# Performance work log

Hardware: AMD Instinct MI355X
Metric: run time of the kernel (lower is better)

The kernel has to match this reference:

```python
import jax, jax.numpy as jnp
import numpy as np

N = 80000   # active voxels
G = 64      # voxel grid side
K = 27      # 3x3x3 kernel taps


def _build_coord_maps():
    """Random unique voxel coords in a G^3 grid; 27-tap neighbor index map (-1 = missing)."""
    rng = np.random.default_rng(0)
    flat = rng.choice(G ** 3, size=N, replace=False).astype(np.int64)
    coords = np.stack(np.unravel_index(flat, (G, G, G)), axis=1)  # (N,3)
    order = np.argsort(flat)
    skeys = flat[order]
    offs = [(dx, dy, dz) for dx in (-1, 0, 1) for dy in (-1, 0, 1) for dz in (-1, 0, 1)]
    nbr = np.full((K, N), -1, np.int32)
    for k, (dx, dy, dz) in enumerate(offs):
        nc = coords + np.array([dx, dy, dz])
        inb = np.all((nc >= 0) & (nc < G), axis=1)
        nkey = nc[:, 0] * G * G + nc[:, 1] * G + nc[:, 2]
        pos = np.clip(np.searchsorted(skeys, nkey), 0, N - 1)
        hit = inb & (skeys[pos] == nkey)
        nbr[k] = np.where(hit, order[pos], -1)
    return nbr


_W_SPECS = [('a1w', (27, 96, 64)), ('a2w', (64, 64)), ('a3w', (27, 64, 64)), ('a4w', (64, 64)),
            ('b1w', (27, 256, 64)), ('b2w', (64, 64)), ('b3w', (27, 64, 32)), ('b4w', (32, 32)),
            ('c1w', (27, 96, 128)), ('c2w', (128, 128)), ('c3w', (128, 128))]
_BN_SPECS = [('a1', 64), ('a2', 64), ('a3', 64), ('a4', 64),
             ('b1', 64), ('b2', 64), ('b3', 32), ('b4', 32),
             ('c1', 128), ('c2', 128), ('c3', 128)]


def setup_inputs() -> dict:
    key = jax.random.key(0)
    ks = jax.random.split(key, 64)
    inp = {
        'feat3d': jax.random.normal(ks[0], (N, 96), jnp.float32),
        'feat2d': jax.random.normal(ks[1], (N, 256), jnp.float32),
    }
    i = 2
    for name, shp in _W_SPECS:
        fan = float(np.prod(shp[:-1]))
        inp[name] = jax.random.normal(ks[i], shp, jnp.float32) * (1.0 / np.sqrt(fan))
        i += 1
    for pre, c in _BN_SPECS:  # folded eval-mode BN: y = x*scale + shift
        inp[pre + 's'] = 1.0 + 0.1 * jax.random.normal(ks[i], (c,), jnp.float32)
        inp[pre + 'b'] = 0.1 * jax.random.normal(ks[i + 1], (c,), jnp.float32)
        i += 2
    inp['nbr_idx'] = jnp.asarray(_build_coord_maps())
    inp['align_idx'] = jnp.arange(N, dtype=jnp.int32)  # 2D/3D share coordinates -> exact match
    return inp


def _sconv(x, W, nbr):
    """Sparse 3x3x3 conv: per-tap masked gather + GEMM, accumulated (gather-GEMM-scatter)."""
    out = jnp.zeros((x.shape[0], W.shape[-1]), x.dtype)
    for k in range(W.shape[0]):
        idx = nbr[k]
        g = jnp.where((idx >= 0)[:, None], x[jnp.maximum(idx, 0)], 0.0)
        out = out + g @ W[k]
    return out


def _bnrelu(x, s, b):
    return jax.nn.relu(x * s + b)


def reference(feat3d, feat2d,
              a1w, a2w, a3w, a4w, b1w, b2w, b3w, b4w, c1w, c2w, c3w,
              a1s, a1b, a2s, a2b, a3s, a3b, a4s, a4b,
              b1s, b1b, b2s, b2b, b3s, b3b, b4s, b4b,
              c1s, c1b, c2s, c2b, c3s, c3b,
              nbr_idx, align_idx):
    # 3D branch: 96 -> 64 (dropout = identity in eval)
    x = _bnrelu(_sconv(feat3d, a1w, nbr_idx), a1s, a1b)
    x = _bnrelu(x @ a2w, a2s, a2b)
    x = _bnrelu(_sconv(x, a3w, nbr_idx), a3s, a3b)
    x3 = _bnrelu(x @ a4w, a4s, a4b)
    # 2D branch: 256 -> 32
    y = _bnrelu(_sconv(feat2d, b1w, nbr_idx), b1s, b1b)
    y = _bnrelu(y @ b2w, b2s, b2b)
    y = _bnrelu(_sconv(y, b3w, nbr_idx), b3s, b3b)
    y2 = _bnrelu(y @ b4w, b4s, b4b)
    # features_at_coordinates: exact-match gather at the 3D coords, NaN/Inf -> 0
    ya = y2[align_idx]
    ya = jnp.where(jnp.isfinite(ya), ya, 0.0)
    # fusion: concat 64+32=96 -> 128
    z = jnp.concatenate([x3, ya], axis=1)
    z = _bnrelu(_sconv(z, c1w, nbr_idx), c1s, c1b)
    z = _bnrelu(z @ c2w, c2s, c2b)
    z = _bnrelu(z @ c3w, c3s, c3b)
    return z
```

## Files before the change

### kernel.cpp

```cpp
#include <hip/hip_runtime.h>

typedef __bf16 bf16;
typedef __bf16 bf16x8 __attribute__((ext_vector_type(8)));
typedef __bf16 bf16x4 __attribute__((ext_vector_type(4)));
typedef float  f32x4  __attribute__((ext_vector_type(4)));

__global__ void f2b_kernel(const float* __restrict__ src, bf16* __restrict__ dst, int n4) {
    int i = blockIdx.x * 256 + threadIdx.x;
    if (i >= n4) return;
    float4 v = ((const float4*)src)[i];
    bf16x4 o = { (bf16)v.x, (bf16)v.y, (bf16)v.z, (bf16)v.w };
    ((bf16x4*)dst)[i] = o;
}

__global__ void swz_kernel(const float* __restrict__ W, bf16* __restrict__ Wf,
                           int cin, int cout, int total) {
    int e = blockIdx.x * 256 + threadIdx.x;
    if (e >= total) return;
    int per_tap = cin * cout;
    int tap = e / per_tap;
    int t2  = e - tap * per_tap;
    int ntc = cout >> 4;
    int s   = t2 / (ntc * 512);
    int r3  = t2 - s * (ntc * 512);
    int nt  = r3 >> 9;
    int L   = (r3 & 511) >> 3;
    int j   = r3 & 7;
    int k   = s * 32 + (L >> 4) * 8 + j;
    int col = nt * 16 + (L & 15);
    Wf[e] = (bf16)W[((size_t)tap * cin + k) * cout + col];
}

template<int CIN, int C1, int TAPS, int KTILE, int C2, int C3>
__global__ __launch_bounds__(256) void layer_kernel(
    const bf16* __restrict__ X,
    const bf16* __restrict__ W1,
    const bf16* __restrict__ W2,
    const bf16* __restrict__ W3,
    const int*  __restrict__ nbr,
    const float* __restrict__ sc1, const float* __restrict__ sh1,
    const float* __restrict__ sc2, const float* __restrict__ sh2,
    const float* __restrict__ sc3, const float* __restrict__ sh3,
    bf16* __restrict__ Y, float* __restrict__ Yf,
    int ystride, int yoff, int n, int nblocks)
{
    constexpr int NT1  = C1 / 16;
    constexpr int KH   = CIN / KTILE;
    constexpr int KS   = KTILE / 32;
    constexpr int CH   = KTILE / 8;
    constexpr int SREG = KTILE / 32;
    constexpr int AST  = KTILE + 8;
    constexpr int WR1  = (C1 >= 64) ? 2 : 1;
    constexpr int WC1  = (C1 == 128) ? 4 : 2;
    constexpr int RG1  = 4 / WR1;
    constexpr int ABUF = 64 * AST;
    constexpr int ABY  = 2 * ABUF * 2;
    constexpr int LS1  = C1 + 8;
    constexpr int LS2  = C2 + 8;
    constexpr int L1BY = 64 * LS1 * 2;
    constexpr int L2BY = (C3 > 0) ? 64 * LS2 * 2 : 0;
    constexpr int SBY  = (ABY > L1BY ? (ABY > L2BY ? ABY : L2BY)
                                     : (L1BY > L2BY ? L1BY : L2BY));

    __shared__ __align__(16) char smem[SBY];
    __shared__ int idxs[TAPS * 64];
    bf16* As = (bf16*)smem;

    const int tid = threadIdx.x;

    {
    }
    const int bq  = nblocks >> 3, br = nblocks & 7;
    const int bx  = blockIdx.x & 7, bs = blockIdx.x >> 3;
    const int sb  = bx * bq + (bx < br ? bx : br) + bs;
    const int base = sb * 64;

    const int lane  = tid & 63;
    const int wv    = tid >> 6;
    const int m16   = lane & 15;
    const int quad  = lane >> 4;
    const int wrow1 = wv % RG1;
    const int wcol1 = wv / RG1;

    for (int e = tid; e < TAPS * 64; e += 256)
        idxs[e] = nbr[(e >> 6) * n + base + (e & 63)];
    __syncthreads();

    int rr[SREG], cof[SREG], lofs[SREG];
#pragma unroll
    for (int j = 0; j < SREG; ++j) {
        int e = tid + 256 * j;
        rr[j]   = e / CH;
        int c   = e - rr[j] * CH;
        cof[j]  = c * 8;
        lofs[j] = rr[j] * AST + c * 8;
    }

    float4 sreg[SREG];
    auto issue_loads = [&](int kh, int t) {
#pragma unroll
        for (int j = 0; j < SREG; ++j) {
            int idx = idxs[t * 64 + rr[j]];
            float4 val = {0.f, 0.f, 0.f, 0.f};
            if (idx >= 0) val = *(const float4*)(X + (size_t)idx * CIN + kh * KTILE + cof[j]);
            sreg[j] = val;
        }
    };
    auto store_lds = [&](int buf) {
#pragma unroll
        for (int j = 0; j < SREG; ++j)
            *(float4*)(&As[buf * ABUF + lofs[j]]) = sreg[j];
    };

    f32x4 acc1[WR1][WC1];
#pragma unroll
    for (int r = 0; r < WR1; ++r)
#pragma unroll
        for (int c = 0; c < WC1; ++c) acc1[r][c] = (f32x4){0.f, 0.f, 0.f, 0.f};

    issue_loads(0, 0);
    store_lds(0);

    int it = 0;
    for (int kh = 0; kh < KH; ++kh)
        for (int t = 0; t < TAPS; ++t, ++it) {
            __syncthreads();

            const bf16* wt = W1 + (size_t)t * (CIN * C1);
            bf16x8 bfr[KS][WC1];
#pragma unroll
            for (int s = 0; s < KS; ++s)
#pragma unroll
                for (int c = 0; c < WC1; ++c)
                    bfr[s][c] = *(const bf16x8*)(wt + ((kh * KS + s) * NT1 + wcol1 * WC1 + c) * 512 + lane * 8);

            int t2 = t + 1, kh2 = kh;
            if (t2 == TAPS) { t2 = 0; kh2 = kh + 1; }
            const bool more = (kh2 < KH);
            if (more) issue_loads(kh2, t2);

            const int buf = it & 1;
#pragma unroll
            for (int s = 0; s < KS; ++s) {
                bf16x8 a[WR1];
#pragma unroll
                for (int r = 0; r < WR1; ++r)
                    a[r] = *(const bf16x8*)(&As[buf * ABUF + ((wrow1 * WR1 + r) * 16 + m16) * AST + s * 32 + quad * 8]);
#pragma unroll
                for (int r = 0; r < WR1; ++r)
#pragma unroll
                    for (int c = 0; c < WC1; ++c)
                        acc1[r][c] = __builtin_amdgcn_mfma_f32_16x16x32_bf16(a[r], bfr[s][c], acc1[r][c], 0, 0, 0);
            }

            if (more) store_lds(buf ^ 1);
        }

    __syncthreads();
    bf16* Lt1 = (bf16*)smem;
#pragma unroll
    for (int c = 0; c < WC1; ++c) {
        int col = (wcol1 * WC1 + c) * 16 + m16;
        float s1 = sc1[col], h1 = sh1[col];
#pragma unroll
        for (int r = 0; r < WR1; ++r) {
            int row0 = (wrow1 * WR1 + r) * 16 + quad * 4;
#pragma unroll
            for (int i = 0; i < 4; ++i) {
                float v = acc1[r][c][i] * s1 + h1;
                v = v > 0.f ? v : 0.f;
                Lt1[(row0 + i) * LS1 + col] = (bf16)v;
            }
        }
    }
    __syncthreads();

    constexpr int NT2 = C2 / 16;
    constexpr int WR2 = (C2 >= 64) ? 2 : 1;
    constexpr int WC2 = (C2 == 128) ? 4 : 2;
    constexpr int RG2 = 4 / WR2;
    constexpr int KS2 = C1 / 32;
    const int wrow2 = wv % RG2, wcol2 = wv / RG2;

    f32x4 acc2[WR2][WC2];
#pragma unroll
    for (int r = 0; r < WR2; ++r)
#pragma unroll
        for (int c = 0; c < WC2; ++c) acc2[r][c] = (f32x4){0.f, 0.f, 0.f, 0.f};

#pragma unroll
    for (int s = 0; s < KS2; ++s) {
        bf16x8 a[WR2], bw[WC2];
#pragma unroll
        for (int r = 0; r < WR2; ++r)
            a[r] = *(const bf16x8*)(&Lt1[((wrow2 * WR2 + r) * 16 + m16) * LS1 + s * 32 + quad * 8]);
#pragma unroll
        for (int c = 0; c < WC2; ++c)
            bw[c] = *(const bf16x8*)(W2 + ((s * NT2 + wcol2 * WC2 + c) * 512 + lane * 8));
#pragma unroll
        for (int r = 0; r < WR2; ++r)
#pragma unroll
            for (int c = 0; c < WC2; ++c)
                acc2[r][c] = __builtin_amdgcn_mfma_f32_16x16x32_bf16(a[r], bw[c], acc2[r][c], 0, 0, 0);
    }

    if constexpr (C3 == 0) {
#pragma unroll
        for (int c = 0; c < WC2; ++c) {
            int col = (wcol2 * WC2 + c) * 16 + m16;
            float s2 = sc2[col], h2 = sh2[col];
#pragma unroll
            for (int r = 0; r < WR2; ++r) {
                int row0 = base + (wrow2 * WR2 + r) * 16 + quad * 4;
#pragma unroll
                for (int i = 0; i < 4; ++i) {
                    float v = acc2[r][c][i] * s2 + h2;
                    v = v > 0.f ? v : 0.f;
                    size_t off = (size_t)(row0 + i) * ystride + yoff + col;
                    if (Yf) Yf[off] = v;
                    else    Y[off] = (bf16)v;
                }
            }
        }
    } else {
        __syncthreads();
        bf16* Lt2 = (bf16*)smem;
#pragma unroll
        for (int c = 0; c < WC2; ++c) {
            int col = (wcol2 * WC2 + c) * 16 + m16;
            float s2 = sc2[col], h2 = sh2[col];
#pragma unroll
            for (int r = 0; r < WR2; ++r) {
                int row0 = (wrow2 * WR2 + r) * 16 + quad * 4;
#pragma unroll
                for (int i = 0; i < 4; ++i) {
                    float v = acc2[r][c][i] * s2 + h2;
                    v = v > 0.f ? v : 0.f;
                    Lt2[(row0 + i) * LS2 + col] = (bf16)v;
                }
            }
        }
        __syncthreads();

        constexpr int C3v = (C3 > 0) ? C3 : 16;
        constexpr int NT3 = C3v / 16;
        constexpr int WR3 = (C3v >= 64) ? 2 : 1;
        constexpr int WC3 = (C3v == 128) ? 4 : 2;
        constexpr int RG3 = 4 / WR3;
        constexpr int KS3 = C2 / 32;
        const int wrow3 = wv % RG3, wcol3 = wv / RG3;

        f32x4 acc3[WR3][WC3];
#pragma unroll
        for (int r = 0; r < WR3; ++r)
#pragma unroll
            for (int c = 0; c < WC3; ++c) acc3[r][c] = (f32x4){0.f, 0.f, 0.f, 0.f};

#pragma unroll
        for (int s = 0; s < KS3; ++s) {
            bf16x8 a[WR3], bw[WC3];
#pragma unroll
            for (int r = 0; r < WR3; ++r)
                a[r] = *(const bf16x8*)(&Lt2[((wrow3 * WR3 + r) * 16 + m16) * LS2 + s * 32 + quad * 8]);
#pragma unroll
            for (int c = 0; c < WC3; ++c)
                bw[c] = *(const bf16x8*)(W3 + ((s * NT3 + wcol3 * WC3 + c) * 512 + lane * 8));
#pragma unroll
            for (int r = 0; r < WR3; ++r)
#pragma unroll
                for (int c = 0; c < WC3; ++c)
                    acc3[r][c] = __builtin_amdgcn_mfma_f32_16x16x32_bf16(a[r], bw[c], acc3[r][c], 0, 0, 0);
        }

#pragma unroll
        for (int c = 0; c < WC3; ++c) {
            int col = (wcol3 * WC3 + c) * 16 + m16;
            float s3 = sc3[col], h3 = sh3[col];
#pragma unroll
            for (int r = 0; r < WR3; ++r) {
                int row0 = base + (wrow3 * WR3 + r) * 16 + quad * 4;
#pragma unroll
                for (int i = 0; i < 4; ++i) {
                    float v = acc3[r][c][i] * s3 + h3;
                    v = v > 0.f ? v : 0.f;
                    size_t off = (size_t)(row0 + i) * ystride + yoff + col;
                    if (Yf) Yf[off] = v;
                    else    Y[off] = (bf16)v;
                }
            }
        }
    }
}

__global__ void concat_kernel(const bf16* __restrict__ y2, const int* __restrict__ align,
                              bf16* __restrict__ z, int n) {
    int e = blockIdx.x * 256 + threadIdx.x;
    if (e >= n * 32) return;
    int i = e >> 5, c = e & 31;
    int a = align[i];
    float v = (float)y2[(size_t)a * 32 + c];
    unsigned u = __builtin_bit_cast(unsigned, v);
    if ((u & 0x7f800000u) == 0x7f800000u) v = 0.f;
    z[(size_t)i * 96 + 64 + c] = (bf16)v;
}

extern "C" void kernel_launch(void* const* d_in, const int* in_sizes, int n_in,
                              void* d_out, int out_size, void* d_ws, size_t ws_size,
                              hipStream_t stream) {
    const float* feat3d = (const float*)d_in[0];
    const float* feat2d = (const float*)d_in[1];
    const float* Wsrc[11];
    for (int i = 0; i < 11; ++i) Wsrc[i] = (const float*)d_in[2 + i];
    const float* bn[22];
    for (int i = 0; i < 22; ++i) bn[i] = (const float*)d_in[13 + i];
    const int* nbr   = (const int*)d_in[35];
    const int* align = (const int*)d_in[36];
    float* out = (float*)d_out;

    const int n = in_sizes[0] / 96;

    char* ws = (char*)d_ws;
    size_t off = 0;
    auto alloc = [&](size_t bytes) -> void* {
        void* p = ws + off;
        off = (off + bytes + 255) & ~(size_t)255;
        return p;
    };
    bf16* F3 = (bf16*)alloc((size_t)n * 96 * 2);
    bf16* F2 = (bf16*)alloc((size_t)n * 256 * 2);
    static const int wt_taps[11] = {27, 1, 27, 1, 27, 1, 27, 1, 27, 1, 1};
    static const int wt_cin[11]  = {96, 64, 64, 64, 256, 64, 64, 32, 96, 128, 128};
    static const int wt_cout[11] = {64, 64, 64, 64, 64, 64, 32, 32, 128, 128, 128};
    bf16* Wf[11];
    for (int i = 0; i < 11; ++i)
        Wf[i] = (bf16*)alloc((size_t)wt_taps[i] * wt_cin[i] * wt_cout[i] * 2);
    bf16* tA = (bf16*)alloc((size_t)n * 64 * 2);
    bf16* tB = (bf16*)alloc((size_t)n * 64 * 2);
    bf16* y2 = (bf16*)alloc((size_t)n * 32 * 2);
    bf16* z  = (bf16*)alloc((size_t)n * 96 * 2);

    f2b_kernel<<<(n * 96 / 4 + 255) / 256, 256, 0, stream>>>(feat3d, F3, n * 96 / 4);
    f2b_kernel<<<(n * 256 / 4 + 255) / 256, 256, 0, stream>>>(feat2d, F2, n * 256 / 4);
    for (int i = 0; i < 11; ++i) {
        int total = wt_taps[i] * wt_cin[i] * wt_cout[i];
        swz_kernel<<<(total + 255) / 256, 256, 0, stream>>>(Wsrc[i], Wf[i], wt_cin[i], wt_cout[i], total);
    }

    const int GB = n / 64;

    layer_kernel<96, 64, 27, 96, 64, 0><<<GB, 256, 0, stream>>>(
        F3, Wf[0], Wf[1], nullptr, nbr,
        bn[0], bn[1], bn[2], bn[3], nullptr, nullptr,
        tB, nullptr, 64, 0, n, GB);
    layer_kernel<64, 64, 27, 64, 64, 0><<<GB, 256, 0, stream>>>(
        tB, Wf[2], Wf[3], nullptr, nbr,
        bn[4], bn[5], bn[6], bn[7], nullptr, nullptr,
        z, nullptr, 96, 0, n, GB);

    layer_kernel<256, 64, 27, 128, 64, 0><<<GB, 256, 0, stream>>>(
        F2, Wf[4], Wf[5], nullptr, nbr,
        bn[8], bn[9], bn[10], bn[11], nullptr, nullptr,
        tA, nullptr, 64, 0, n, GB);
    layer_kernel<64, 32, 27, 64, 32, 0><<<GB, 256, 0, stream>>>(
        tA, Wf[6], Wf[7], nullptr, nbr,
        bn[12], bn[13], bn[14], bn[15], nullptr, nullptr,
        y2, nullptr, 32, 0, n, GB);

    concat_kernel<<<(n * 32 + 255) / 256, 256, 0, stream>>>(y2, align, z, n);

    layer_kernel<96, 128, 27, 96, 128, 128><<<GB, 256, 0, stream>>>(
        z, Wf[8], Wf[9], Wf[10], nbr,
        bn[16], bn[17], bn[18], bn[19], bn[20], bn[21],
        nullptr, out, 128, 0, n, GB);
}
```

Measured before the change: 593.9 us.

## Gather sparse-conv inputs straight into MFMA fragments and enlarge row tiles

The main loop no longer stages gathered neighbour rows through double-buffered LDS with a barrier every tap. Each wave now loads its bf16x8 A and B fragments directly from global memory into registers, with register double-buffering over a flattened tap×K-chunk loop. Most layers also switch from 64-row to 128-row blocks, so each block reuses the per-tap weight fragments over more rows. In exchange, waves that share rows load the same A data again (relying on cache hits), gathers are narrower per load, and register pressure rises.

```diff
diff --git a/kernel.cpp b/kernel.cpp
--- a/kernel.cpp
+++ b/kernel.cpp
@@ -31,7 +31,7 @@
     Wf[e] = (bf16)W[((size_t)tap * cin + k) * cout + col];
 }
 
-template<int CIN, int C1, int TAPS, int KTILE, int C2, int C3>
+template<int CIN, int C1, int TAPS, int C2, int C3, int ROWS>
 __global__ __launch_bounds__(256) void layer_kernel(
     const bf16* __restrict__ X,
     const bf16* __restrict__ W1,
@@ -44,120 +44,87 @@
     bf16* __restrict__ Y, float* __restrict__ Yf,
     int ystride, int yoff, int n, int nblocks)
 {
-    constexpr int NT1  = C1 / 16;
-    constexpr int KH   = CIN / KTILE;
-    constexpr int KS   = KTILE / 32;
-    constexpr int CH   = KTILE / 8;
-    constexpr int SREG = KTILE / 32;
-    constexpr int AST  = KTILE + 8;
-    constexpr int WR1  = (C1 >= 64) ? 2 : 1;
-    constexpr int WC1  = (C1 == 128) ? 4 : 2;
-    constexpr int RG1  = 4 / WR1;
-    constexpr int ABUF = 64 * AST;
-    constexpr int ABY  = 2 * ABUF * 2;
-    constexpr int LS1  = C1 + 8;
-    constexpr int LS2  = C2 + 8;
-    constexpr int L1BY = 64 * LS1 * 2;
-    constexpr int L2BY = (C3 > 0) ? 64 * LS2 * 2 : 0;
-    constexpr int SBY  = (ABY > L1BY ? (ABY > L2BY ? ABY : L2BY)
-                                     : (L1BY > L2BY ? L1BY : L2BY));
-
-    __shared__ __align__(16) char smem[SBY];
-    __shared__ int idxs[TAPS * 64];
-    bf16* As = (bf16*)smem;
+    constexpr int KH  = CIN / 32;
+    constexpr int NT1 = C1 / 16;
+    constexpr int CG1 = (C1 == 128) ? 4 : 2;
+    constexpr int WC1 = NT1 / CG1;
+    constexpr int RG1 = 4 / CG1;
+    constexpr int WR1 = ROWS / 16 / RG1;
+    constexpr int TOTAL = KH * TAPS;
+    constexpr int LS1 = C1 + 8;
+    constexpr int LS2 = C2 + 8;
+    constexpr int TILE_E = (C3 > 0)
+        ? (ROWS * LS1 > ROWS * LS2 ? ROWS * LS1 : ROWS * LS2)
+        : ROWS * LS1;
+
+    __shared__ int idxs[TAPS * ROWS];
+    __shared__ __align__(16) bf16 tile[TILE_E];
 
     const int tid = threadIdx.x;
 
-    {
-    }
-    const int bq  = nblocks >> 3, br = nblocks & 7;
-    const int bx  = blockIdx.x & 7, bs = blockIdx.x >> 3;
-    const int sb  = bx * bq + (bx < br ? bx : br) + bs;
-    const int base = sb * 64;
-
-    const int lane  = tid & 63;
-    const int wv    = tid >> 6;
-    const int m16   = lane & 15;
-    const int quad  = lane >> 4;
+    const int bq = nblocks >> 3, br = nblocks & 7;
+    const int bx = blockIdx.x & 7, bs = blockIdx.x >> 3;
+    const int sb = bx * bq + (bx < br ? bx : br) + bs;
+    const int base = sb * ROWS;
+
+    const int lane = tid & 63;
+    const int wv   = tid >> 6;
+    const int m16  = lane & 15;
+    const int quad = lane >> 4;
     const int wrow1 = wv % RG1;
     const int wcol1 = wv / RG1;
-
-    for (int e = tid; e < TAPS * 64; e += 256)
-        idxs[e] = nbr[(e >> 6) * n + base + (e & 63)];
+    const int r0 = wrow1 * WR1 * 16 + m16;
+
+    for (int e = tid; e < TAPS * ROWS; e += 256)
+        idxs[e] = nbr[(e / ROWS) * n + base + (e % ROWS)];
     __syncthreads();
 
-    int rr[SREG], cof[SREG], lofs[SREG];
-#pragma unroll
-    for (int j = 0; j < SREG; ++j) {
-        int e = tid + 256 * j;
-        rr[j]   = e / CH;
-        int c   = e - rr[j] * CH;
-        cof[j]  = c * 8;
-        lofs[j] = rr[j] * AST + c * 8;
-    }
-
-    float4 sreg[SREG];
-    auto issue_loads = [&](int kh, int t) {
-#pragma unroll
-        for (int j = 0; j < SREG; ++j) {
-            int idx = idxs[t * 64 + rr[j]];
-            float4 val = {0.f, 0.f, 0.f, 0.f};
-            if (idx >= 0) val = *(const float4*)(X + (size_t)idx * CIN + kh * KTILE + cof[j]);
-            sreg[j] = val;
+    f32x4 acc1[WR1][WC1];
+#pragma unroll
+    for (int r = 0; r < WR1; ++r)
+#pragma unroll
+        for (int c = 0; c < WC1; ++c) acc1[r][c] = (f32x4){0.f, 0.f, 0.f, 0.f};
+
+    const bf16 z0 = (bf16)0.f;
+    const int boff = wcol1 * WC1 * 512 + lane * 8;
+    const int koff = quad * 8;
+
+    bf16x8 Acur[WR1], Bcur[WC1], Anxt[WR1], Bnxt[WC1];
+
+    auto load_frags = [&](int it, bf16x8 (&A)[WR1], bf16x8 (&B)[WC1]) {
+        int t = it % TAPS, kh = it / TAPS;
+        const bf16* wt = W1 + ((size_t)t * KH + kh) * (NT1 * 512) + boff;
+#pragma unroll
+        for (int c = 0; c < WC1; ++c)
+            B[c] = *(const bf16x8*)(wt + c * 512);
+#pragma unroll
+        for (int r = 0; r < WR1; ++r) {
+            int idx = idxs[t * ROWS + r0 + r * 16];
+            bf16x8 a = {z0, z0, z0, z0, z0, z0, z0, z0};
+            if (idx >= 0)
+                a = *(const bf16x8*)(X + (size_t)idx * CIN + kh * 32 + koff);
+            A[r] = a;
         }
     };
-    auto store_lds = [&](int buf) {
-#pragma unroll
-        for (int j = 0; j < SREG; ++j)
-            *(float4*)(&As[buf * ABUF + lofs[j]]) = sreg[j];
+    auto do_mfma = [&](bf16x8 (&A)[WR1], bf16x8 (&B)[WC1]) {
+#pragma unroll
+        for (int r = 0; r < WR1; ++r)
+#pragma unroll
+            for (int c = 0; c < WC1; ++c)
+                acc1[r][c] = __builtin_amdgcn_mfma_f32_16x16x32_bf16(A[r], B[c], acc1[r][c], 0, 0, 0);
     };
 
-    f32x4 acc1[WR1][WC1];
-#pragma unroll
-    for (int r = 0; r < WR1; ++r)
-#pragma unroll
-        for (int c = 0; c < WC1; ++c) acc1[r][c] = (f32x4){0.f, 0.f, 0.f, 0.f};
-
-    issue_loads(0, 0);
-    store_lds(0);
-
+    load_frags(0, Acur, Bcur);
     int it = 0;
-    for (int kh = 0; kh < KH; ++kh)
-        for (int t = 0; t < TAPS; ++t, ++it) {
-            __syncthreads();
-
-            const bf16* wt = W1 + (size_t)t * (CIN * C1);
-            bf16x8 bfr[KS][WC1];
-#pragma unroll
-            for (int s = 0; s < KS; ++s)
-#pragma unroll
-                for (int c = 0; c < WC1; ++c)
-                    bfr[s][c] = *(const bf16x8*)(wt + ((kh * KS + s) * NT1 + wcol1 * WC1 + c) * 512 + lane * 8);
-
-            int t2 = t + 1, kh2 = kh;
-            if (t2 == TAPS) { t2 = 0; kh2 = kh + 1; }
-            const bool more = (kh2 < KH);
-            if (more) issue_loads(kh2, t2);
-
-            const int buf = it & 1;
-#pragma unroll
-            for (int s = 0; s < KS; ++s) {
-                bf16x8 a[WR1];
-#pragma unroll
-                for (int r = 0; r < WR1; ++r)
-                    a[r] = *(const bf16x8*)(&As[buf * ABUF + ((wrow1 * WR1 + r) * 16 + m16) * AST + s * 32 + quad * 8]);
-#pragma unroll
-                for (int r = 0; r < WR1; ++r)
-#pragma unroll
-                    for (int c = 0; c < WC1; ++c)
-                        acc1[r][c] = __builtin_amdgcn_mfma_f32_16x16x32_bf16(a[r], bfr[s][c], acc1[r][c], 0, 0, 0);
-            }
-
-            if (more) store_lds(buf ^ 1);
-        }
-
-    __syncthreads();
-    bf16* Lt1 = (bf16*)smem;
+    while (true) {
+        if (it + 1 < TOTAL) load_frags(it + 1, Anxt, Bnxt);
+        do_mfma(Acur, Bcur);
+        ++it; if (it == TOTAL) break;
+        if (it + 1 < TOTAL) load_frags(it + 1, Acur, Bcur);
+        do_mfma(Anxt, Bnxt);
+        ++it; if (it == TOTAL) break;
+    }
+
 #pragma unroll
     for (int c = 0; c < WC1; ++c) {
         int col = (wcol1 * WC1 + c) * 16 + m16;
@@ -169,16 +136,17 @@
             for (int i = 0; i < 4; ++i) {
                 float v = acc1[r][c][i] * s1 + h1;
                 v = v > 0.f ? v : 0.f;
-                Lt1[(row0 + i) * LS1 + col] = (bf16)v;
+                tile[(row0 + i) * LS1 + col] = (bf16)v;
             }
         }
     }
     __syncthreads();
 
     constexpr int NT2 = C2 / 16;
-    constexpr int WR2 = (C2 >= 64) ? 2 : 1;
-    constexpr int WC2 = (C2 == 128) ? 4 : 2;
-    constexpr int RG2 = 4 / WR2;
+    constexpr int CG2 = (C2 == 128) ? 4 : 2;
+    constexpr int WC2 = NT2 / CG2;
+    constexpr int RG2 = 4 / CG2;
+    constexpr int WR2 = ROWS / 16 / RG2;
     constexpr int KS2 = C1 / 32;
     const int wrow2 = wv % RG2, wcol2 = wv / RG2;
 
@@ -193,7 +161,7 @@
         bf16x8 a[WR2], bw[WC2];
 #pragma unroll
         for (int r = 0; r < WR2; ++r)
-            a[r] = *(const bf16x8*)(&Lt1[((wrow2 * WR2 + r) * 16 + m16) * LS1 + s * 32 + quad * 8]);
+            a[r] = *(const bf16x8*)(&tile[((wrow2 * WR2 + r) * 16 + m16) * LS1 + s * 32 + quad * 8]);
 #pragma unroll
         for (int c = 0; c < WC2; ++c)
             bw[c] = *(const bf16x8*)(W2 + ((s * NT2 + wcol2 * WC2 + c) * 512 + lane * 8));
@@ -224,7 +192,6 @@
         }
     } else {
         __syncthreads();
-        bf16* Lt2 = (bf16*)smem;
 #pragma unroll
         for (int c = 0; c < WC2; ++c) {
             int col = (wcol2 * WC2 + c) * 16 + m16;
@@ -236,7 +203,7 @@
                 for (int i = 0; i < 4; ++i) {
                     float v = acc2[r][c][i] * s2 + h2;
                     v = v > 0.f ? v : 0.f;
-                    Lt2[(row0 + i) * LS2 + col] = (bf16)v;
+                    tile[(row0 + i) * LS2 + col] = (bf16)v;
                 }
             }
         }
@@ -244,9 +211,10 @@
 
         constexpr int C3v = (C3 > 0) ? C3 : 16;
         constexpr int NT3 = C3v / 16;
-        constexpr int WR3 = (C3v >= 64) ? 2 : 1;
-        constexpr int WC3 = (C3v == 128) ? 4 : 2;
-        constexpr int RG3 = 4 / WR3;
+        constexpr int CG3 = (C3v == 128) ? 4 : 2;
+        constexpr int WC3 = NT3 / CG3;
+        constexpr int RG3 = 4 / CG3;
+        constexpr int WR3 = ROWS / 16 / RG3;
         constexpr int KS3 = C2 / 32;
         const int wrow3 = wv % RG3, wcol3 = wv / RG3;
 
@@ -261,7 +229,7 @@
             bf16x8 a[WR3], bw[WC3];
 #pragma unroll
             for (int r = 0; r < WR3; ++r)
-                a[r] = *(const bf16x8*)(&Lt2[((wrow3 * WR3 + r) * 16 + m16) * LS2 + s * 32 + quad * 8]);
+                a[r] = *(const bf16x8*)(&tile[((wrow3 * WR3 + r) * 16 + m16) * LS2 + s * 32 + quad * 8]);
 #pragma unroll
             for (int c = 0; c < WC3; ++c)
                 bw[c] = *(const bf16x8*)(W3 + ((s * NT3 + wcol3 * WC3 + c) * 512 + lane * 8));
@@ -346,30 +314,31 @@
         swz_kernel<<<(total + 255) / 256, 256, 0, stream>>>(Wsrc[i], Wf[i], wt_cin[i], wt_cout[i], total);
     }
 
-    const int GB = n / 64;
-
-    layer_kernel<96, 64, 27, 96, 64, 0><<<GB, 256, 0, stream>>>(
+    const int GB128 = n / 128;
+    const int GB64  = n / 64;
+
+    layer_kernel<96, 64, 27, 64, 0, 128><<<GB128, 256, 0, stream>>>(
         F3, Wf[0], Wf[1], nullptr, nbr,
         bn[0], bn[1], bn[2], bn[3], nullptr, nullptr,
-        tB, nullptr, 64, 0, n, GB);
-    layer_kernel<64, 64, 27, 64, 64, 0><<<GB, 256, 0, stream>>>(
+        tB, nullptr, 64, 0, n, GB128);
+    layer_kernel<64, 64, 27, 64, 0, 128><<<GB128, 256, 0, stream>>>(
         tB, Wf[2], Wf[3], nullptr, nbr,
         bn[4], bn[5], bn[6], bn[7], nullptr, nullptr,
-        z, nullptr, 96, 0, n, GB);
-
-    layer_kernel<256, 64, 27, 128, 64, 0><<<GB, 256, 0, stream>>>(
+        z, nullptr, 96, 0, n, GB128);
+
+    layer_kernel<256, 64, 27, 64, 0, 128><<<GB128, 256, 0, stream>>>(
         F2, Wf[4], Wf[5], nullptr, nbr,
         bn[8], bn[9], bn[10], bn[11], nullptr, nullptr,
-        tA, nullptr, 64, 0, n, GB);
-    layer_kernel<64, 32, 27, 64, 32, 0><<<GB, 256, 0, stream>>>(
+        tA, nullptr, 64, 0, n, GB128);
+    layer_kernel<64, 32, 27, 32, 0, 128><<<GB128, 256, 0, stream>>>(
         tA, Wf[6], Wf[7], nullptr, nbr,
         bn[12], bn[13], bn[14], bn[15], nullptr, nullptr,
-        y2, nullptr, 32, 0, n, GB);
+        y2, nullptr, 32, 0, n, GB128);
 
     concat_kernel<<<(n * 32 + 255) / 256, 256, 0, stream>>>(y2, align, z, n);
 
-    layer_kernel<96, 128, 27, 96, 128, 128><<<GB, 256, 0, stream>>>(
+    layer_kernel<96, 128, 27, 128, 128, 64><<<GB64, 256, 0, stream>>>(
         z, Wf[8], Wf[9], Wf[10], nbr,
         bn[16], bn[17], bn[18], bn[19], bn[20], bn[21],
-        nullptr, out, 128, 0, n, GB);
-}
+        nullptr, out, 128, 0, n, GB64);
+}
```

New measurement: 684.6 us. 1.15x slower.
